# Kernel optimization log

Hardware: AMD Instinct MI355X
Metric: run time of the kernel (lower is better)

## Reference

```python
import jax, jax.numpy as jnp
import numpy as np

NUM_NODE = 40000
DIM = 100
LAYERS = 2
ALPHA = 0.2
B, N = 128, 70
E = 640000
STDV = 1.0 / np.sqrt(DIM)  # reset_parameters uniform(-stdv, stdv)


def setup_inputs() -> dict:
    key = jax.random.key(0)
    ks = jax.random.split(key, 16)
    inputs = jax.random.randint(ks[0], (B, N), 0, NUM_NODE, dtype=jnp.int32)
    edge_matrix = jax.random.randint(ks[1], (B, N, N), 0, 5, dtype=jnp.int32)
    mask = jnp.ones((B, N), dtype=jnp.int32)
    reversed_sess_item = jax.random.randint(ks[2], (B, N), 0, NUM_NODE + 1, dtype=jnp.int32)
    sess_item = jax.random.randint(ks[3], (B, N), 0, NUM_NODE + 1, dtype=jnp.int32)
    D = jax.random.uniform(ks[4], (B, B), dtype=jnp.float32) / B  # degree-norm scale
    A = jax.random.uniform(ks[5], (B, B), dtype=jnp.float32)
    sess_len = jnp.full((B, 1), float(N), dtype=jnp.float32)
    embedding = jax.random.uniform(ks[6], (NUM_NODE, DIM), jnp.float32, -STDV, STDV)
    a_0 = jax.random.uniform(ks[7], (DIM,), jnp.float32, -STDV, STDV)
    a_1 = jax.random.uniform(ks[8], (DIM,), jnp.float32, -STDV, STDV)
    a_2 = jax.random.uniform(ks[9], (DIM,), jnp.float32, -STDV, STDV)
    a_3 = jax.random.uniform(ks[10], (DIM,), jnp.float32, -STDV, STDV)
    adj_rows = jax.random.randint(ks[11], (E,), 0, NUM_NODE, dtype=jnp.int32)
    adj_cols = jax.random.randint(ks[12], (E,), 0, NUM_NODE, dtype=jnp.int32)
    adj_vals = jax.random.uniform(ks[13], (E,), dtype=jnp.float32) * 0.1
    return dict(inputs=inputs, edge_matrix=edge_matrix, mask=mask,
                reversed_sess_item=reversed_sess_item, sess_item=sess_item,
                D=D, A=A, sess_len=sess_len, embedding=embedding,
                a_0=a_0, a_1=a_1, a_2=a_2, a_3=a_3,
                adj_rows=adj_rows, adj_cols=adj_cols, adj_vals=adj_vals)


def _leaky(x):
    return jnp.where(x >= 0, x, ALPHA * x)


def _intra(h, adj, a_vecs):
    # a_input[b,i,j] = h[b,i]*h[b,j]; e_k = leaky(a_input @ a_k)
    # = leaky((h*a_k) @ h^T) -- avoids materializing [B,N,N,D]
    e = [_leaky(jnp.einsum('bid,bjd->bij', h * a, h)) for a in a_vecs]
    neg = jnp.full_like(e[0], -9e15)
    alpha = jnp.where(adj == 1, e[0], neg)
    alpha = jnp.where(adj == 2, e[1], alpha)
    alpha = jnp.where(adj == 3, e[2], alpha)
    alpha = jnp.where(adj == 4, e[3], alpha)
    alpha = jax.nn.softmax(alpha, axis=-1)
    return jnp.einsum('bij,bjd->bid', alpha, h)


def _inter(embedding, rows, cols, vals):
    x = embedding
    acc = x
    for _ in range(LAYERS):
        x = jax.ops.segment_sum(vals[:, None] * x[cols], rows, num_segments=NUM_NODE)
        acc = acc + x
    return acc / (LAYERS + 1)


def _session(embedding, D, A, sess_item, sess_len):
    emb_pad = jnp.concatenate([jnp.zeros((1, DIM), embedding.dtype), embedding], 0)
    seq_h = emb_pad[sess_item]                       # [B, N, D]
    s = jnp.sum(seq_h, axis=1) / sess_len            # [B, D]
    DA = D @ A
    acc = s
    for _ in range(LAYERS):
        s = DA @ s
        acc = acc + s
    return acc / (LAYERS + 1)


def reference(inputs, edge_matrix, mask, reversed_sess_item, sess_item,
              D, A, sess_len, embedding, a_0, a_1, a_2, a_3,
              adj_rows, adj_cols, adj_vals):
    h = embedding[inputs]                            # [B, N, D]
    intra_item_emb = _intra(h, edge_matrix, (a_0, a_1, a_2, a_3))
    inter_item_emb = _inter(embedding, adj_rows, adj_cols, adj_vals)
    session_emb = _session(embedding, D, A, sess_item, sess_len)
    inter_pad = jnp.concatenate([jnp.zeros((1, DIM), embedding.dtype), inter_item_emb], 0)
    seq_h = inter_pad[sess_item]                     # [B, N, D]
    # dropout_local/global = 0 (eval mode)
    output = intra_item_emb + seq_h
    return output, session_emb
```

## Files before the change

### kernel.cpp

```cpp
#include <hip/hip_runtime.h>
#include <hip/hip_bf16.h>
#include <hip/hip_fp8.h>

#define NUM_NODE 40000
#define DIM 100
#define NBATCH 128
#define NSEQ 70
#define NEDGE 640000
#define LEAKY_ALPHA 0.2f
#define RPB 18
#define CAP 64
#define HCAP 32
#define HB 52
#define CNTSTRIDE 16
#define NSLICE 8
#define SLICE_ROWS 5000

__device__ __forceinline__ float bf2f(unsigned short u) {
    return __uint_as_float(((unsigned int)u) << 16);
}
__device__ __forceinline__ unsigned short f2bf(float f) {
    unsigned int u = __float_as_uint(f);
    return (unsigned short)((u + 0x7FFFu + ((u >> 16) & 1u)) >> 16);
}
__device__ __forceinline__ float lo16(unsigned int u) { return __uint_as_float(u << 16); }
__device__ __forceinline__ float hi16(unsigned int u) { return __uint_as_float(u & 0xffff0000u); }

__device__ __forceinline__ unsigned int f2q(float f) {
    __hip_fp8_e4m3 q(f);
    return (unsigned int)*reinterpret_cast<unsigned char*>(&q);
}
__device__ __forceinline__ float q2f(unsigned int b) {
    __hip_fp8_e4m3 q;
    *reinterpret_cast<unsigned char*>(&q) = (unsigned char)(b & 0xffu);
    return (float)q;
}

#define INIT_BLOCKS 3907

__global__ __launch_bounds__(256) void init_kernel(
    const float* __restrict__ emb, unsigned int* __restrict__ emb8,
    int4* __restrict__ cntp_v4, int* __restrict__ nlist)
{
    int gid = blockIdx.x * 256 + threadIdx.x;
    if (gid == 0) *nlist = 0;
    if (gid < NUM_NODE * DIM / 4) {
        float4 v = reinterpret_cast<const float4*>(emb)[gid];
        emb8[gid] = f2q(v.x) | (f2q(v.y) << 8) | (f2q(v.z) << 16) | (f2q(v.w) << 24);
    }
    if (gid < NUM_NODE * CNTSTRIDE / 4)
        cntp_v4[gid] = make_int4(0, 0, 0, 0);
}

#define TAIL_BLOCKS 256
#define BUILD_CHUNKS 625

__global__ __launch_bounds__(256) void build_kernel(
    const int* __restrict__ rows, const int* __restrict__ cols,
    const float* __restrict__ vals, int* __restrict__ cntp,
    int2* __restrict__ edata,
    const int* __restrict__ sess_item,
    int* __restrict__ nlist, int* __restrict__ list,
    const float* __restrict__ emb, const float* __restrict__ sess_len,
    const float* __restrict__ Dm, const float* __restrict__ Am,
    float* __restrict__ s, float* __restrict__ DA)
{
    if (blockIdx.x < TAIL_BLOCKS) {
        __shared__ float part[2][128];
        int tid = threadIdx.x;
        int half = tid >> 7, t = tid & 127;
        int task = blockIdx.x;
        if (task < NBATCH) {
            float acc = 0.f;
            if (t < DIM) {
                int n0 = half * 35;
                #pragma unroll 5
                for (int n = n0; n < n0 + 35; ++n) {
                    int r = sess_item[task * NSEQ + n];
                    int rr = (r > 0) ? (r - 1) : 0;
                    float m = (r > 0) ? 1.f : 0.f;
                    acc += m * emb[(size_t)rr * DIM + t];
                }
            }
            part[half][t] = acc;
            __syncthreads();
            if (half == 0 && t < DIM)
                s[task * DIM + t] = (part[0][t] + part[1][t]) / sess_len[task];
        } else {
            int i = task - NBATCH;
            float acc = 0.f;
            int k0 = half * 64;
            #pragma unroll 4
            for (int k = k0; k < k0 + 64; ++k)
                acc += Dm[i * NBATCH + k] * Am[k * NBATCH + t];
            part[half][t] = acc;
            __syncthreads();
            if (half == 0)
                DA[i * NBATCH + t] = part[0][t] + part[1][t];
        }
        return;
    }
    int blk = blockIdx.x - TAIL_BLOCKS;
    int g = blk & (NSLICE - 1);
    int chunk = blk >> 3;
    int tid = threadIdx.x;
    if (g == 0) {
        int idx = chunk * 256 + tid;
        if (idx < NBATCH * NSEQ) {
            int r = sess_item[idx];
            if (r > 0 && atomicExch(&cntp[(r - 1) * CNTSTRIDE + 4], 1) == 0)
                list[atomicAdd(nlist, 1)] = r - 1;
        }
    }
    int base_e = (chunk * 256 + tid) * 4;
    int rlo = g * SLICE_ROWS;
    int4 r4 = *reinterpret_cast<const int4*>(rows + base_e);
    #pragma unroll
    for (int i = 0; i < 4; ++i) {
        int e = base_e + i;
        int r = (i == 0) ? r4.x : (i == 1) ? r4.y : (i == 2) ? r4.z : r4.w;
        unsigned int rr = (unsigned int)(r - rlo);
        if (rr < SLICE_ROWS) {
            int half = (e >= NEDGE / 2);
            int pos = atomicAdd(&cntp[r * CNTSTRIDE + half], 1);
            if (pos < HCAP)
                edata[(size_t)r * CAP + half * HCAP + pos] =
                    make_int2(cols[e], __float_as_int(vals[e]));
        }
    }
}

__device__ __forceinline__ void bucket_accum_fp8(
    const int2* __restrict__ ep, int deg, const unsigned int* __restrict__ x8,
    int c, float& a0, float& a1, float& a2, float& a3)
{
    int e = 0;
    for (; e + 4 <= deg; e += 4) {
        int4 p0 = *reinterpret_cast<const int4*>(ep + e);
        int4 p1 = *reinterpret_cast<const int4*>(ep + e + 2);
        unsigned int w0 = x8[(size_t)p0.x * 25 + c];
        unsigned int w1 = x8[(size_t)p0.z * 25 + c];
        unsigned int w2 = x8[(size_t)p1.x * 25 + c];
        unsigned int w3 = x8[(size_t)p1.z * 25 + c];
        float v0 = __int_as_float(p0.y), v1 = __int_as_float(p0.w);
        float v2 = __int_as_float(p1.y), v3 = __int_as_float(p1.w);
        a0 += v0 * q2f(w0) + v1 * q2f(w1) + v2 * q2f(w2) + v3 * q2f(w3);
        a1 += v0 * q2f(w0 >> 8) + v1 * q2f(w1 >> 8) + v2 * q2f(w2 >> 8) + v3 * q2f(w3 >> 8);
        a2 += v0 * q2f(w0 >> 16) + v1 * q2f(w1 >> 16) + v2 * q2f(w2 >> 16) + v3 * q2f(w3 >> 16);
        a3 += v0 * q2f(w0 >> 24) + v1 * q2f(w1 >> 24) + v2 * q2f(w2 >> 24) + v3 * q2f(w3 >> 24);
    }
    for (; e < deg; ++e) {
        int2 ed = ep[e];
        float v = __int_as_float(ed.y);
        unsigned int w = x8[(size_t)ed.x * 25 + c];
        a0 += v * q2f(w);
        a1 += v * q2f(w >> 8);
        a2 += v * q2f(w >> 16);
        a3 += v * q2f(w >> 24);
    }
}

#define SPMM_BLOCKS 3907
#define SESS_TAIL 50

__global__ __launch_bounds__(256) void spmm1_sprop_kernel(
    const int* __restrict__ cntp, const int2* __restrict__ edata,
    const unsigned int* __restrict__ emb8,
    unsigned short* __restrict__ y1, unsigned int* __restrict__ y18,
    const float* __restrict__ DA, const float* __restrict__ s,
    float* __restrict__ s1)
{
    if (blockIdx.x >= SPMM_BLOCKS) {
        int idx = (blockIdx.x - SPMM_BLOCKS) * 256 + threadIdx.x;
        int i = idx / DIM, d = idx - i * DIM;
        if (i >= NBATCH) return;
        float acc = 0.f;
        #pragma unroll 8
        for (int k = 0; k < NBATCH; ++k) acc += DA[i * NBATCH + k] * s[k * DIM + d];
        s1[i * DIM + d] = acc;
        return;
    }
    int gid = blockIdx.x * 256 + threadIdx.x;
    int r = gid / 25;
    int c = gid - r * 25;
    if (r >= NUM_NODE) return;
    float a0 = 0.f, a1 = 0.f, a2 = 0.f, a3 = 0.f;
    int d0 = cntp[r * CNTSTRIDE];     if (d0 > HCAP) d0 = HCAP;
    int d1 = cntp[r * CNTSTRIDE + 1]; if (d1 > HCAP) d1 = HCAP;
    const int2* ep = edata + (size_t)r * CAP;
    bucket_accum_fp8(ep, d0, emb8, c, a0, a1, a2, a3);
    bucket_accum_fp8(ep + HCAP, d1, emb8, c, a0, a1, a2, a3);
    ushort4 o;
    o.x = f2bf(a0); o.y = f2bf(a1); o.z = f2bf(a2); o.w = f2bf(a3);
    *reinterpret_cast<ushort4*>(y1 + (size_t)r * DIM + c * 4) = o;
    y18[(size_t)r * 25 + c] = f2q(a0) | (f2q(a1) << 8) | (f2q(a2) << 16) | (f2q(a3) << 24);
}

#define SPMM2_BLOCKS 875

__global__ __launch_bounds__(256) void spmm2_final_kernel(
    const int* __restrict__ cntp, const int2* __restrict__ edata,
    const unsigned int* __restrict__ y18, unsigned short* __restrict__ y2,
    const int* __restrict__ nlist, const int* __restrict__ list,
    const float* __restrict__ DA, const float* __restrict__ s,
    const float* __restrict__ s1, float* __restrict__ out2)
{
    if (blockIdx.x >= SPMM2_BLOCKS) {
        int idx = (blockIdx.x - SPMM2_BLOCKS) * 256 + threadIdx.x;
        int i = idx / DIM, d = idx - i * DIM;
        if (i >= NBATCH) return;
        float acc = 0.f;
        #pragma unroll 8
        for (int k = 0; k < NBATCH; ++k) acc += DA[i * NBATCH + k] * s1[k * DIM + d];
        int o = i * DIM + d;
        out2[o] = (s[o] + s1[o] + acc) * (1.f / 3.f);
        return;
    }
    int gid = blockIdx.x * 256 + threadIdx.x;
    int li = gid / 25;
    int c = gid - li * 25;
    if (li >= *nlist) return;
    int r = list[li];
    float a0 = 0.f, a1 = 0.f, a2 = 0.f, a3 = 0.f;
    int d0 = cntp[r * CNTSTRIDE];     if (d0 > HCAP) d0 = HCAP;
    int d1 = cntp[r * CNTSTRIDE + 1]; if (d1 > HCAP) d1 = HCAP;
    const int2* ep = edata + (size_t)r * CAP;
    bucket_accum_fp8(ep, d0, y18, c, a0, a1, a2, a3);
    bucket_accum_fp8(ep + HCAP, d1, y18, c, a0, a1, a2, a3);
    ushort4 o;
    o.x = f2bf(a0); o.y = f2bf(a1); o.z = f2bf(a2); o.w = f2bf(a3);
    *reinterpret_cast<ushort4*>(y2 + (size_t)r * DIM + c * 4) = o;
}

__global__ __launch_bounds__(1024) void intra_kernel(
    const int* __restrict__ inputs, const int* __restrict__ edge,
    const int* __restrict__ sess_item,
    const float* __restrict__ emb,
    const unsigned short* __restrict__ y1, const unsigned short* __restrict__ y2,
    const float* __restrict__ a0, const float* __restrict__ a1,
    const float* __restrict__ a2, const float* __restrict__ a3,
    float* __restrict__ out)
{
    __shared__ unsigned int hb[NSEQ][HB];
    __shared__ unsigned int avb[4][HB];
    __shared__ float al[RPB][NSEQ + 2];
    int b = blockIdx.x >> 2;
    int q = blockIdx.x & 3;
    int i0 = q * RPB;
    int nrows = (i0 + RPB <= NSEQ) ? RPB : (NSEQ - i0);
    int tid = threadIdx.x;

    for (int idx = tid; idx < NSEQ * 25; idx += 1024) {
        int n = idx / 25, p = idx - n * 25;
        float4 v = *reinterpret_cast<const float4*>(
            emb + (size_t)inputs[b * NSEQ + n] * DIM + p * 4);
        hb[n][p * 2]     = (unsigned int)f2bf(v.x) | ((unsigned int)f2bf(v.y) << 16);
        hb[n][p * 2 + 1] = (unsigned int)f2bf(v.z) | ((unsigned int)f2bf(v.w) << 16);
    }
    if (tid < 4 * 50) {
        int k = tid / 50, u = tid - k * 50;
        const float* ap = (k == 0) ? a0 : (k == 1) ? a1 : (k == 2) ? a2 : a3;
        unsigned int lo = f2bf(ap[2 * u]);
        unsigned int hi = f2bf(ap[2 * u + 1]);
        avb[k][u] = lo | (hi << 16);
    }
    __syncthreads();

    for (int p = tid; p < nrows * NSEQ; p += 1024) {
        int il = p / NSEQ, j = p - il * NSEQ;
        int i = i0 + il;
        int em = edge[(size_t)b * NSEQ * NSEQ + i * NSEQ + j];
        float val = -9e15f;
        if (em >= 1 && em <= 4) {
            const unsigned int* hi_ = hb[i];
            const unsigned int* hj_ = hb[j];
            const unsigned int* ab_ = avb[em - 1];
            float s0 = 0.f, s1_ = 0.f, s2 = 0.f, s3 = 0.f;
            #pragma unroll
            for (int u = 0; u < 48; u += 4) {
                uint4 x1 = *reinterpret_cast<const uint4*>(hi_ + u);
                uint4 x2 = *reinterpret_cast<const uint4*>(hj_ + u);
                uint4 x3 = *reinterpret_cast<const uint4*>(ab_ + u);
                s0 += lo16(x1.x) * lo16(x2.x) * lo16(x3.x);
                s1_ += hi16(x1.x) * hi16(x2.x) * hi16(x3.x);
                s2 += lo16(x1.y) * lo16(x2.y) * lo16(x3.y);
                s3 += hi16(x1.y) * hi16(x2.y) * hi16(x3.y);
                s0 += lo16(x1.z) * lo16(x2.z) * lo16(x3.z);
                s1_ += hi16(x1.z) * hi16(x2.z) * hi16(x3.z);
                s2 += lo16(x1.w) * lo16(x2.w) * lo16(x3.w);
                s3 += hi16(x1.w) * hi16(x2.w) * hi16(x3.w);
            }
            {
                uint2 x1 = *reinterpret_cast<const uint2*>(hi_ + 48);
                uint2 x2 = *reinterpret_cast<const uint2*>(hj_ + 48);
                uint2 x3 = *reinterpret_cast<const uint2*>(ab_ + 48);
                s0 += lo16(x1.x) * lo16(x2.x) * lo16(x3.x);
                s1_ += hi16(x1.x) * hi16(x2.x) * hi16(x3.x);
                s2 += lo16(x1.y) * lo16(x2.y) * lo16(x3.y);
                s3 += hi16(x1.y) * hi16(x2.y) * hi16(x3.y);
            }
            float sd = (s0 + s1_) + (s2 + s3);
            val = sd >= 0.f ? sd : LEAKY_ALPHA * sd;
        }
        al[il][j] = val;
    }
    __syncthreads();

    int wid = tid >> 6, lane = tid & 63;
    for (int row = wid; row < nrows; row += 16) {
        float v0 = (lane < NSEQ) ? al[row][lane] : -INFINITY;
        float v1 = (lane + 64 < NSEQ) ? al[row][lane + 64] : -INFINITY;
        float m = fmaxf(v0, v1);
        #pragma unroll
        for (int off = 32; off >= 1; off >>= 1) m = fmaxf(m, __shfl_xor(m, off, 64));
        float e0 = (lane < NSEQ) ? __expf(v0 - m) : 0.f;
        float e1 = (lane + 64 < NSEQ) ? __expf(v1 - m) : 0.f;
        float ssum = e0 + e1;
        #pragma unroll
        for (int off = 32; off >= 1; off >>= 1) ssum += __shfl_xor(ssum, off, 64);
        float inv = 1.f / ssum;
        if (lane < NSEQ) al[row][lane] = e0 * inv;
        if (lane + 64 < NSEQ) al[row][lane + 64] = e1 * inv;
    }
    __syncthreads();

    if (tid < nrows * 25) {
        int il = tid / 25, chunk = tid - il * 25;
        int i = i0 + il;
        int u = chunk * 2;
        float4 acc = make_float4(0.f, 0.f, 0.f, 0.f);
        for (int j = 0; j < NSEQ; ++j) {
            float w = al[il][j];
            uint2 hv = *reinterpret_cast<const uint2*>(hb[j] + u);
            acc.x += w * lo16(hv.x);
            acc.y += w * hi16(hv.x);
            acc.z += w * lo16(hv.y);
            acc.w += w * hi16(hv.y);
        }
        int dc = chunk * 4;
        int r = sess_item[b * NSEQ + i];
        if (r > 0) {
            size_t o = (size_t)(r - 1) * DIM + dc;
            float4 ev = *reinterpret_cast<const float4*>(emb + o);
            ushort4 u1 = *reinterpret_cast<const ushort4*>(y1 + o);
            ushort4 u2 = *reinterpret_cast<const ushort4*>(y2 + o);
            acc.x += (ev.x + bf2f(u1.x) + bf2f(u2.x)) * (1.f / 3.f);
            acc.y += (ev.y + bf2f(u1.y) + bf2f(u2.y)) * (1.f / 3.f);
            acc.z += (ev.z + bf2f(u1.z) + bf2f(u2.z)) * (1.f / 3.f);
            acc.w += (ev.w + bf2f(u1.w) + bf2f(u2.w)) * (1.f / 3.f);
        }
        *reinterpret_cast<float4*>(out + (size_t)b * NSEQ * DIM + (size_t)i * DIM + dc) = acc;
    }
}

extern "C" void kernel_launch(void* const* d_in, const int* in_sizes, int n_in,
                              void* d_out, int out_size, void* d_ws, size_t ws_size,
                              hipStream_t stream) {
    const int*   inputs    = (const int*)d_in[0];
    const int*   edge      = (const int*)d_in[1];
    const int*   sess_item = (const int*)d_in[4];
    const float* Dm        = (const float*)d_in[5];
    const float* Am        = (const float*)d_in[6];
    const float* sess_len  = (const float*)d_in[7];
    const float* emb       = (const float*)d_in[8];
    const float* a0        = (const float*)d_in[9];
    const float* a1        = (const float*)d_in[10];
    const float* a2        = (const float*)d_in[11];
    const float* a3        = (const float*)d_in[12];
    const int*   arows     = (const int*)d_in[13];
    const int*   acols     = (const int*)d_in[14];
    const float* avals     = (const float*)d_in[15];

    float* out      = (float*)d_out;
    float* out_sess = out + (size_t)NBATCH * NSEQ * DIM;

    char* ws = (char*)d_ws;
    unsigned int*   emb8 = (unsigned int*)ws;
    unsigned short* y1   = (unsigned short*)(ws + 4000000);
    unsigned int*   y18  = (unsigned int*)(ws + 12000000);
    unsigned short* y2   = (unsigned short*)(ws + 16000000);
    char*  base2 = ws + 24000000;
    float* s        = (float*)(base2 + 0);
    float* DA       = (float*)(base2 + 65536);
    float* s1       = (float*)(base2 + 2 * 65536);
    int*   cntp     = (int*)(base2 + 3 * 65536);
    int*   nlist    = (int*)(base2 + 3 * 65536 + 2560000);
    int*   list     = (int*)(base2 + 3 * 65536 + 2560000 + 64);
    int2*  edata    = (int2*)(base2 + 3 * 65536 + 2560000 + 64 + 36864);

    init_kernel<<<INIT_BLOCKS, 256, 0, stream>>>(emb, emb8, (int4*)cntp, nlist);

    build_kernel<<<TAIL_BLOCKS + NSLICE * BUILD_CHUNKS, 256, 0, stream>>>(
        arows, acols, avals, cntp, edata, sess_item, nlist, list,
        emb, sess_len, Dm, Am, s, DA);

    spmm1_sprop_kernel<<<SPMM_BLOCKS + SESS_TAIL, 256, 0, stream>>>(
        cntp, edata, emb8, y1, y18, DA, s, s1);

    spmm2_final_kernel<<<SPMM2_BLOCKS + SESS_TAIL, 256, 0, stream>>>(
        cntp, edata, y18, y2, nlist, list, DA, s, s1, out_sess);

    intra_kernel<<<NBATCH * 4, 1024, 0, stream>>>(inputs, edge, sess_item,
                                                  emb, y1, y2, a0, a1, a2, a3, out);
}
```

Measured before the change: 97.55 us.

## Store propagated embeddings only in fp8 and move emb quantization into build kernel

The bf16 copies of the first and second propagation layers are dropped. The intra kernel now reads the fp8 y18 and a new fp8 y28 buffer when forming the final output. The fp32-to-fp8 conversion of the embedding table moves from the init kernel into the build kernel's edge blocks, which shrinks init to zeroing counters only. This removes one bf16 write stream per SpMM pass and makes the intra kernel's gather narrower. In exchange, the inter-item embedding added to the output carries fp8 precision, which may push error closer to tolerance.

```diff
diff --git a/kernel.cpp b/kernel.cpp
--- a/kernel.cpp
+++ b/kernel.cpp
@@ -36,20 +36,14 @@
     return (float)q;
 }
 
-#define INIT_BLOCKS 3907
-
-__global__ __launch_bounds__(256) void init_kernel(
-    const float* __restrict__ emb, unsigned int* __restrict__ emb8,
-    int4* __restrict__ cntp_v4, int* __restrict__ nlist)
+#define INIT_BLOCKS 625
+
+__global__ __launch_bounds__(256) void init_kernel(int4* __restrict__ cntp_v4,
+                                                   int* __restrict__ nlist)
 {
     int gid = blockIdx.x * 256 + threadIdx.x;
     if (gid == 0) *nlist = 0;
-    if (gid < NUM_NODE * DIM / 4) {
-        float4 v = reinterpret_cast<const float4*>(emb)[gid];
-        emb8[gid] = f2q(v.x) | (f2q(v.y) << 8) | (f2q(v.z) << 16) | (f2q(v.w) << 24);
-    }
-    if (gid < NUM_NODE * CNTSTRIDE / 4)
-        cntp_v4[gid] = make_int4(0, 0, 0, 0);
+    cntp_v4[gid] = make_int4(0, 0, 0, 0);
 }
 
 #define TAIL_BLOCKS 256
@@ -61,7 +55,8 @@
     int2* __restrict__ edata,
     const int* __restrict__ sess_item,
     int* __restrict__ nlist, int* __restrict__ list,
-    const float* __restrict__ emb, const float* __restrict__ sess_len,
+    const float* __restrict__ emb, unsigned int* __restrict__ emb8,
+    const float* __restrict__ sess_len,
     const float* __restrict__ Dm, const float* __restrict__ Am,
     float* __restrict__ s, float* __restrict__ DA)
 {
@@ -101,9 +96,14 @@
         return;
     }
     int blk = blockIdx.x - TAIL_BLOCKS;
+    int tid = threadIdx.x;
+    int gid = blk * 256 + tid;
+    if (gid < NUM_NODE * DIM / 4) {
+        float4 v = reinterpret_cast<const float4*>(emb)[gid];
+        emb8[gid] = f2q(v.x) | (f2q(v.y) << 8) | (f2q(v.z) << 16) | (f2q(v.w) << 24);
+    }
     int g = blk & (NSLICE - 1);
     int chunk = blk >> 3;
-    int tid = threadIdx.x;
     if (g == 0) {
         int idx = chunk * 256 + tid;
         if (idx < NBATCH * NSEQ) {
@@ -165,8 +165,7 @@
 
 __global__ __launch_bounds__(256) void spmm1_sprop_kernel(
     const int* __restrict__ cntp, const int2* __restrict__ edata,
-    const unsigned int* __restrict__ emb8,
-    unsigned short* __restrict__ y1, unsigned int* __restrict__ y18,
+    const unsigned int* __restrict__ emb8, unsigned int* __restrict__ y18,
     const float* __restrict__ DA, const float* __restrict__ s,
     float* __restrict__ s1)
 {
@@ -190,9 +189,6 @@
     const int2* ep = edata + (size_t)r * CAP;
     bucket_accum_fp8(ep, d0, emb8, c, a0, a1, a2, a3);
     bucket_accum_fp8(ep + HCAP, d1, emb8, c, a0, a1, a2, a3);
-    ushort4 o;
-    o.x = f2bf(a0); o.y = f2bf(a1); o.z = f2bf(a2); o.w = f2bf(a3);
-    *reinterpret_cast<ushort4*>(y1 + (size_t)r * DIM + c * 4) = o;
     y18[(size_t)r * 25 + c] = f2q(a0) | (f2q(a1) << 8) | (f2q(a2) << 16) | (f2q(a3) << 24);
 }
 
@@ -200,7 +196,7 @@
 
 __global__ __launch_bounds__(256) void spmm2_final_kernel(
     const int* __restrict__ cntp, const int2* __restrict__ edata,
-    const unsigned int* __restrict__ y18, unsigned short* __restrict__ y2,
+    const unsigned int* __restrict__ y18, unsigned int* __restrict__ y28,
     const int* __restrict__ nlist, const int* __restrict__ list,
     const float* __restrict__ DA, const float* __restrict__ s,
     const float* __restrict__ s1, float* __restrict__ out2)
@@ -227,16 +223,14 @@
     const int2* ep = edata + (size_t)r * CAP;
     bucket_accum_fp8(ep, d0, y18, c, a0, a1, a2, a3);
     bucket_accum_fp8(ep + HCAP, d1, y18, c, a0, a1, a2, a3);
-    ushort4 o;
-    o.x = f2bf(a0); o.y = f2bf(a1); o.z = f2bf(a2); o.w = f2bf(a3);
-    *reinterpret_cast<ushort4*>(y2 + (size_t)r * DIM + c * 4) = o;
+    y28[(size_t)r * 25 + c] = f2q(a0) | (f2q(a1) << 8) | (f2q(a2) << 16) | (f2q(a3) << 24);
 }
 
 __global__ __launch_bounds__(1024) void intra_kernel(
     const int* __restrict__ inputs, const int* __restrict__ edge,
     const int* __restrict__ sess_item,
     const float* __restrict__ emb,
-    const unsigned short* __restrict__ y1, const unsigned short* __restrict__ y2,
+    const unsigned int* __restrict__ y18, const unsigned int* __restrict__ y28,
     const float* __restrict__ a0, const float* __restrict__ a1,
     const float* __restrict__ a2, const float* __restrict__ a3,
     float* __restrict__ out)
@@ -340,14 +334,15 @@
         int dc = chunk * 4;
         int r = sess_item[b * NSEQ + i];
         if (r > 0) {
-            size_t o = (size_t)(r - 1) * DIM + dc;
+            int rr = r - 1;
+            size_t o = (size_t)rr * DIM + dc;
             float4 ev = *reinterpret_cast<const float4*>(emb + o);
-            ushort4 u1 = *reinterpret_cast<const ushort4*>(y1 + o);
-            ushort4 u2 = *reinterpret_cast<const ushort4*>(y2 + o);
-            acc.x += (ev.x + bf2f(u1.x) + bf2f(u2.x)) * (1.f / 3.f);
-            acc.y += (ev.y + bf2f(u1.y) + bf2f(u2.y)) * (1.f / 3.f);
-            acc.z += (ev.z + bf2f(u1.z) + bf2f(u2.z)) * (1.f / 3.f);
-            acc.w += (ev.w + bf2f(u1.w) + bf2f(u2.w)) * (1.f / 3.f);
+            unsigned int u1 = y18[(size_t)rr * 25 + chunk];
+            unsigned int u2 = y28[(size_t)rr * 25 + chunk];
+            acc.x += (ev.x + q2f(u1)       + q2f(u2))       * (1.f / 3.f);
+            acc.y += (ev.y + q2f(u1 >> 8)  + q2f(u2 >> 8))  * (1.f / 3.f);
+            acc.z += (ev.z + q2f(u1 >> 16) + q2f(u2 >> 16)) * (1.f / 3.f);
+            acc.w += (ev.w + q2f(u1 >> 24) + q2f(u2 >> 24)) * (1.f / 3.f);
         }
         *reinterpret_cast<float4*>(out + (size_t)b * NSEQ * DIM + (size_t)i * DIM + dc) = acc;
     }
@@ -375,11 +370,10 @@
     float* out_sess = out + (size_t)NBATCH * NSEQ * DIM;
 
     char* ws = (char*)d_ws;
-    unsigned int*   emb8 = (unsigned int*)ws;
-    unsigned short* y1   = (unsigned short*)(ws + 4000000);
-    unsigned int*   y18  = (unsigned int*)(ws + 12000000);
-    unsigned short* y2   = (unsigned short*)(ws + 16000000);
-    char*  base2 = ws + 24000000;
+    unsigned int* emb8 = (unsigned int*)ws;
+    unsigned int* y18  = (unsigned int*)(ws + 4000000);
+    unsigned int* y28  = (unsigned int*)(ws + 8000000);
+    char*  base2 = ws + 12000000;
     float* s        = (float*)(base2 + 0);
     float* DA       = (float*)(base2 + 65536);
     float* s1       = (float*)(base2 + 2 * 65536);
@@ -388,18 +382,18 @@
     int*   list     = (int*)(base2 + 3 * 65536 + 2560000 + 64);
     int2*  edata    = (int2*)(base2 + 3 * 65536 + 2560000 + 64 + 36864);
 
-    init_kernel<<<INIT_BLOCKS, 256, 0, stream>>>(emb, emb8, (int4*)cntp, nlist);
+    init_kernel<<<INIT_BLOCKS, 256, 0, stream>>>((int4*)cntp, nlist);
 
     build_kernel<<<TAIL_BLOCKS + NSLICE * BUILD_CHUNKS, 256, 0, stream>>>(
         arows, acols, avals, cntp, edata, sess_item, nlist, list,
-        emb, sess_len, Dm, Am, s, DA);
+        emb, emb8, sess_len, Dm, Am, s, DA);
 
     spmm1_sprop_kernel<<<SPMM_BLOCKS + SESS_TAIL, 256, 0, stream>>>(
-        cntp, edata, emb8, y1, y18, DA, s, s1);
+        cntp, edata, emb8, y18, DA, s, s1);
 
     spmm2_final_kernel<<<SPMM2_BLOCKS + SESS_TAIL, 256, 0, stream>>>(
-        cntp, edata, y18, y2, nlist, list, DA, s, s1, out_sess);
+        cntp, edata, y18, y28, nlist, list, DA, s, s1, out_sess);
 
     intra_kernel<<<NBATCH * 4, 1024, 0, stream>>>(inputs, edge, sess_item,
-                                                  emb, y1, y2, a0, a1, a2, a3, out);
-}
+                                                  emb, y18, y28, a0, a1, a2, a3, out);
+}
```

After: 97.41 us. About the same (-0.1%).
